# Optimization experiments

Measured on AMD Instinct MI355X. Metric: run time of the kernel, lower is better.

## Reference

```python
import jax, jax.numpy as jnp
import numpy as np

B, S, D_IN, D_H = 8, 2048, 512, 512

def setup_inputs() -> dict:
    key = jax.random.key(0)
    ks = jax.random.split(key, 7)
    scale = 1.0 / np.sqrt(D_IN)
    return {
        "x": jax.random.normal(ks[0], (B, S, D_IN), dtype=jnp.float32),
        "Wq": jax.random.uniform(ks[1], (D_IN, D_H), jnp.float32, -scale, scale),
        "bq": jax.random.uniform(ks[2], (D_H,), jnp.float32, -scale, scale),
        "Wk": jax.random.uniform(ks[3], (D_IN, D_H), jnp.float32, -scale, scale),
        "bk": jax.random.uniform(ks[4], (D_H,), jnp.float32, -scale, scale),
        "Wv": jax.random.uniform(ks[5], (D_IN, D_H), jnp.float32, -scale, scale),
        "bv": jax.random.uniform(ks[6], (D_H,), jnp.float32, -scale, scale),
    }

def reference(x, Wq, bq, Wk, bk, Wv, bv):
    q = jnp.einsum("bsd,dh->bsh", x, Wq) + bq  # [B,S,H]
    k = jnp.einsum("bsd,dh->bsh", x, Wk) + bk
    v = jnp.einsum("bsd,dh->bsh", x, Wv) + bv
    # NOTE: original has NO 1/sqrt(d) scaling — faithful reproduction
    scores = jnp.einsum("bqh,bkh->bqk", q, k)  # [B,S,S]
    probs = jax.nn.softmax(scores, axis=-1)
    return jnp.einsum("bqk,bkh->bqh", probs, v)
```

## Files before the change

kernel.cpp:

```cpp
#include <hip/hip_runtime.h>


typedef __attribute__((ext_vector_type(8))) _Float16 f16x8;
typedef __attribute__((ext_vector_type(8))) short bf16x8;
typedef __attribute__((ext_vector_type(4))) float f32x4;

__device__ __forceinline__ unsigned short f2h(float f) {
  _Float16 h = (_Float16)f;
  return *(unsigned short*)&h;
}
__device__ __forceinline__ unsigned short f2bf(float f) {
  unsigned int u = __float_as_uint(f);
  unsigned int r = (u + 0x7fffu + ((u >> 16) & 1u)) >> 16;
  return (unsigned short)r;
}
__device__ __forceinline__ float bf2f(unsigned short h) {
  return __uint_as_float(((unsigned int)h) << 16);
}

__device__ __forceinline__ void load_lds16(const void* g, void* l) {
  __builtin_amdgcn_global_load_lds(
      (const __attribute__((address_space(1))) unsigned int*)g,
      (__attribute__((address_space(3))) unsigned int*)l, 16, 0, 0);
}

__global__ __launch_bounds__(256) void convx_kernel(const float* __restrict__ x,
                                                    unsigned short* __restrict__ xh) {
  int i = blockIdx.x * 256 + threadIdx.x;
  float4 v = ((const float4*)x)[i];
  union { unsigned short h[4]; short4 s4; } u;
  u.h[0] = f2h(v.x); u.h[1] = f2h(v.y); u.h[2] = f2h(v.z); u.h[3] = f2h(v.w);
  ((short4*)xh)[i] = u.s4;
}

__global__ __launch_bounds__(256) void convw_kernel(
    const float* __restrict__ W0, const float* __restrict__ W1,
    const float* __restrict__ W2, unsigned short* __restrict__ Wt) {
  const float* W = (blockIdx.z == 0) ? W0 : (blockIdx.z == 1) ? W1 : W2;
  unsigned short* t = Wt + (size_t)blockIdx.z * 512 * 512;
  __shared__ float tile[32][33];
  int tx = threadIdx.x, ty = threadIdx.y;
  int h0 = blockIdx.x * 32, d0 = blockIdx.y * 32;
  for (int i = ty; i < 32; i += 8) tile[i][tx] = W[(long)(d0 + i) * 512 + h0 + tx];
  __syncthreads();
  for (int i = ty; i < 32; i += 8)
    t[(long)(h0 + i) * 512 + d0 + tx] = f2h(tile[tx][i]);
}

__global__ __launch_bounds__(256) void gemm_qkv_kernel(
    const unsigned short* __restrict__ A,
    const unsigned short* __restrict__ Bt,
    unsigned short* __restrict__ Qo, unsigned short* __restrict__ Ko,
    unsigned short* __restrict__ VTo,
    const float* __restrict__ bq, const float* __restrict__ bk,
    const float* __restrict__ bv) {
  __shared__ alignas(16) unsigned short As[128 * 32];
  __shared__ alignas(16) unsigned short Bs[128 * 32];
  const int t = threadIdx.x;
  const long long bm = (long long)blockIdx.x * 128;
  const long long bn = (long long)blockIdx.y * 128;

  const int ar = t >> 2;
  const int ac = (t & 3) * 8;

  f32x4 acc[4][4];
#pragma unroll
  for (int i = 0; i < 4; i++)
#pragma unroll
    for (int j = 0; j < 4; j++) acc[i][j] = {0.f, 0.f, 0.f, 0.f};

  const int lane = t & 63;
  const int wave = t >> 6;
  const int wm = (wave & 1) * 64;
  const int wn = (wave >> 1) * 64;
  const int fm = lane & 15;
  const int k8 = (lane >> 4) * 8;

  for (int kt = 0; kt < 512; kt += 32) {
#pragma unroll
    for (int r = 0; r < 2; r++)
      load_lds16(A + (bm + r * 64 + ar) * 512 + kt + ac, &As[r * 2048 + t * 8]);
#pragma unroll
    for (int r = 0; r < 2; r++)
      load_lds16(Bt + (bn + r * 64 + ar) * 512 + kt + ac, &Bs[r * 2048 + t * 8]);
    __syncthreads();

    f16x8 af[4], bfr[4];
#pragma unroll
    for (int i = 0; i < 4; i++)
      af[i] = *(const f16x8*)&As[(wm + i * 16 + fm) * 32 + k8];
#pragma unroll
    for (int j = 0; j < 4; j++)
      bfr[j] = *(const f16x8*)&Bs[(wn + j * 16 + fm) * 32 + k8];
#pragma unroll
    for (int i = 0; i < 4; i++)
#pragma unroll
      for (int j = 0; j < 4; j++)
        acc[i][j] = __builtin_amdgcn_mfma_f32_16x16x32_f16(af[i], bfr[j], acc[i][j], 0, 0, 0);
    __syncthreads();
  }

  const int crow = (lane >> 4) * 4;
  const int ccol = lane & 15;
#pragma unroll
  for (int j = 0; j < 4; j++) {
    const long long col = bn + wn + j * 16 + ccol;
    float bias = (col < 512) ? bq[col] : (col < 1024) ? bk[col - 512] : bv[col - 1024];
#pragma unroll
    for (int i = 0; i < 4; i++) {
      const long long row0 = bm + wm + i * 16 + crow;
      if (col >= 1024) {
        const long long b = row0 >> 11;
        const long long s = row0 & 2047;
        const long long dcol = col - 1024;
        union { unsigned short h[4]; short4 s4; } u;
#pragma unroll
        for (int r = 0; r < 4; r++) u.h[r] = f2bf(acc[i][j][r] + bias);
        const long long unit = b * 64 + (s >> 5);
        const int L = ((int)dcol * 64 + (int)(s & 31) * 2) ^ ((((int)dcol >> 1) & 7) << 4);
        *(short4*)((char*)VTo + unit * 32768 + L) = u.s4;
      } else {
        unsigned short* dst = (col < 512) ? (Qo + row0 * 512 + col)
                                          : (Ko + row0 * 512 + (col - 512));
#pragma unroll
        for (int r = 0; r < 4; r++) dst[(size_t)r * 512] = f2h(acc[i][j][r] + bias);
      }
    }
  }
}

__global__ __launch_bounds__(512, 2) void attn_fused_kernel(
    const unsigned short* __restrict__ Qg,
    const unsigned short* __restrict__ Kg,
    const unsigned short* __restrict__ Vt,
    float* __restrict__ out) {
  __shared__ alignas(16) unsigned short SB[2][16384];
  __shared__ alignas(16) unsigned short Qh[16384];
  __shared__ alignas(16) unsigned short Ps[8192];
  __shared__ float rsw[4][64];

  const int t = threadIdx.x;
  const int lane = t & 63;
  const int w = t >> 6;
  const int fm = lane & 15;
  const int g = lane >> 4;
  const int qh = w & 1;
  const int kg = w >> 1;
  const int b = blockIdx.x & 7;
  const int q0 = (blockIdx.x >> 3) << 6;

  const unsigned short* Qb = Qg + ((size_t)b * 2048 + q0) * 512;
  const unsigned short* Kb = Kg + (size_t)b * 2048 * 512;
  const unsigned short* Vb = Vt + (size_t)b * 2048 * 512;

  int ksrc[4], qsrc[4]; unsigned int sdst[4];
#pragma unroll
  for (int r = 0; r < 4; ++r) {
    const int L = r * 8192 + t * 16;
    sdst[r] = L >> 1;
    const int kr = L >> 8;
    ksrc[r] = kr * 512 + (((L & 255) ^ ((kr & 7) << 4)) >> 1);
    const int qr = L >> 9;
    qsrc[r] = qr * 512 + (((L & 511) ^ ((qr & 7) << 4)) >> 1);
  }

#pragma unroll
  for (int r = 0; r < 4; ++r) load_lds16(Qb + qsrc[r], &SB[0][sdst[r]]);
#pragma unroll
  for (int r = 0; r < 4; ++r) load_lds16(Qb + 256 + qsrc[r], &Qh[sdst[r]]);
  asm volatile("s_waitcnt vmcnt(4)" ::: "memory");
  __builtin_amdgcn_s_barrier();

  const int swz = (fm & 7) << 4;
  const int vswz = ((fm >> 1) & 7) << 4;
  f16x8 qf[2][8];
#pragma unroll
  for (int j = 0; j < 2; ++j)
#pragma unroll
    for (int ds = 0; ds < 8; ++ds)
      qf[j][ds] = *(const f16x8*)((const char*)SB[0] +
          (qh * 32 + j * 16 + fm) * 512 + ((g * 16 + ds * 64) ^ swz));
  asm volatile("s_waitcnt lgkmcnt(0)" ::: "memory");
  __builtin_amdgcn_s_barrier();
#pragma unroll
  for (int r = 0; r < 4; ++r) load_lds16(Kb + ksrc[r], &SB[0][sdst[r]]);

  f32x4 oacc[2][8];
#pragma unroll
  for (int i = 0; i < 2; ++i)
#pragma unroll
    for (int jj = 0; jj < 8; ++jj) oacc[i][jj] = {0.f, 0.f, 0.f, 0.f};
  float psum0 = 0.f, psum1 = 0.f;
  f32x4 sacc[2][2];

  for (int kt = 0; kt < 16; ++kt) {
    const size_t kbase = (size_t)kt * 65536;
#pragma unroll
    for (int u = 0; u < 8; ++u) {
      unsigned short* cur = SB[u & 1];
      unsigned short* nxt = SB[(u & 1) ^ 1];
      if (u < 3) {
#pragma unroll
        for (int r = 0; r < 4; ++r)
          load_lds16(Kb + kbase + (u + 1) * 128 + ksrc[r], &nxt[sdst[r]]);
      } else if (u < 7) {
        const unsigned short* vs = Vb + (size_t)(kt * 4 + (u - 3)) * 16384;
#pragma unroll
        for (int r = 0; r < 4; ++r) load_lds16(vs + sdst[r], &nxt[sdst[r]]);
      } else if (kt < 15) {
#pragma unroll
        for (int r = 0; r < 4; ++r)
          load_lds16(Kb + kbase + 65536 + ksrc[r], &nxt[sdst[r]]);
      }
      if (kt == 15 && u == 7)
        asm volatile("s_waitcnt vmcnt(0)" ::: "memory");
      else
        asm volatile("s_waitcnt vmcnt(4)" ::: "memory");
      __builtin_amdgcn_s_barrier();
      __builtin_amdgcn_sched_barrier(0);

      __builtin_amdgcn_s_setprio(1);
      if (u < 4) {
        if (u == 0) {
          sacc[0][0] = {0.f, 0.f, 0.f, 0.f}; sacc[0][1] = {0.f, 0.f, 0.f, 0.f};
          sacc[1][0] = {0.f, 0.f, 0.f, 0.f}; sacc[1][1] = {0.f, 0.f, 0.f, 0.f};
        }
#pragma unroll
        for (int s = 0; s < 4; ++s) {
          const f16x8 a0 = *(const f16x8*)((const char*)cur +
              (kg * 32 + fm) * 256 + ((g * 16 + s * 64) ^ swz));
          const f16x8 a1 = *(const f16x8*)((const char*)cur +
              (kg * 32 + 16 + fm) * 256 + ((g * 16 + s * 64) ^ swz));
          f16x8 b0, b1;
          if (u < 2) {
            b0 = qf[0][u * 4 + s]; b1 = qf[1][u * 4 + s];
          } else {
            const int dz = (g * 16 + ((u - 2) * 4 + s) * 64) ^ swz;
            b0 = *(const f16x8*)((const char*)Qh + (qh * 32 + fm) * 512 + dz);
            b1 = *(const f16x8*)((const char*)Qh + (qh * 32 + 16 + fm) * 512 + dz);
          }
          sacc[0][0] = __builtin_amdgcn_mfma_f32_16x16x32_f16(a0, b0, sacc[0][0], 0, 0, 0);
          sacc[0][1] = __builtin_amdgcn_mfma_f32_16x16x32_f16(a0, b1, sacc[0][1], 0, 0, 0);
          sacc[1][0] = __builtin_amdgcn_mfma_f32_16x16x32_f16(a1, b0, sacc[1][0], 0, 0, 0);
          sacc[1][1] = __builtin_amdgcn_mfma_f32_16x16x32_f16(a1, b1, sacc[1][1], 0, 0, 0);
        }
        if (u == 3) {
#pragma unroll
          for (int i = 0; i < 2; ++i)
#pragma unroll
            for (int j = 0; j < 2; ++j) {
              const int q = qh * 32 + j * 16 + fm;
              const int k2 = (kg * 32 + i * 16 + g * 4) * 2;
              union { unsigned short h[4]; short4 s4; } uu;
              float s0 = 0.f;
#pragma unroll
              for (int r = 0; r < 4; ++r) {
                const unsigned short pb = f2bf(__expf(sacc[i][j][r]));
                uu.h[r] = pb; s0 += bf2f(pb);
              }
              if (j == 0) psum0 += s0; else psum1 += s0;
              *(short4*)((char*)Ps + q * 256 + (k2 ^ swz)) = uu.s4;
            }
        }
      } else {
        const int ju = u - 4;
        const bf16x8 p0 = *(const bf16x8*)((const char*)Ps +
            (qh * 32 + fm) * 256 + ((ju * 64 + g * 16) ^ swz));
        const bf16x8 p1 = *(const bf16x8*)((const char*)Ps +
            (qh * 32 + 16 + fm) * 256 + ((ju * 64 + g * 16) ^ swz));
#pragma unroll
        for (int jj = 0; jj < 8; ++jj) {
          const bf16x8 vf = *(const bf16x8*)((const char*)cur +
              ((((kg * 128 + jj * 16 + fm) * 64) + g * 16) ^ vswz));
          oacc[0][jj] = __builtin_amdgcn_mfma_f32_16x16x32_bf16(p0, vf, oacc[0][jj], 0, 0, 0);
          oacc[1][jj] = __builtin_amdgcn_mfma_f32_16x16x32_bf16(p1, vf, oacc[1][jj], 0, 0, 0);
        }
      }
      __builtin_amdgcn_s_setprio(0);
      asm volatile("s_waitcnt lgkmcnt(0)" ::: "memory");
      __builtin_amdgcn_s_barrier();
    }
  }

  psum0 += __shfl_xor(psum0, 16); psum0 += __shfl_xor(psum0, 32);
  psum1 += __shfl_xor(psum1, 16); psum1 += __shfl_xor(psum1, 32);
  if (g == 0) {
    rsw[kg][qh * 32 + fm] = psum0;
    rsw[kg][qh * 32 + 16 + fm] = psum1;
  }
  __syncthreads();

  float* ob = out + ((size_t)b * 2048 + q0) * 512;
#pragma unroll
  for (int i = 0; i < 2; ++i) {
    float inv[4];
#pragma unroll
    for (int r = 0; r < 4; ++r) {
      const int q = qh * 32 + i * 16 + g * 4 + r;
      inv[r] = 1.0f / (rsw[0][q] + rsw[1][q] + rsw[2][q] + rsw[3][q]);
    }
#pragma unroll
    for (int jj = 0; jj < 8; ++jj) {
      const int d = kg * 128 + jj * 16 + fm;
#pragma unroll
      for (int r = 0; r < 4; ++r)
        ob[(size_t)(qh * 32 + i * 16 + g * 4 + r) * 512 + d] = oacc[i][jj][r] * inv[r];
    }
  }
}

extern "C" void kernel_launch(void* const* d_in, const int* in_sizes, int n_in,
                              void* d_out, int out_size, void* d_ws, size_t ws_size,
                              hipStream_t stream) {
  const float* x  = (const float*)d_in[0];
  const float* Wq = (const float*)d_in[1];
  const float* bq = (const float*)d_in[2];
  const float* Wk = (const float*)d_in[3];
  const float* bk = (const float*)d_in[4];
  const float* Wv = (const float*)d_in[5];
  const float* bv = (const float*)d_in[6];
  float* out = (float*)d_out;

  const size_t SZ = (size_t)16384 * 512 * 2;
  char* p = (char*)d_ws;
  unsigned short* xh = (unsigned short*)p; p += SZ;
  unsigned short* Wt = (unsigned short*)p; p += (size_t)3 * 512 * 512 * 2;
  unsigned short* Qb = (unsigned short*)p; p += SZ;
  unsigned short* Kb = (unsigned short*)p; p += SZ;
  unsigned short* VT = (unsigned short*)p; p += SZ;

  convx_kernel<<<8192, 256, 0, stream>>>(x, xh);
  convw_kernel<<<dim3(16, 16, 3), dim3(32, 8), 0, stream>>>(Wq, Wk, Wv, Wt);
  gemm_qkv_kernel<<<dim3(128, 12), 256, 0, stream>>>(xh, Wt, Qb, Kb, VT, bq, bk, bv);
  attn_fused_kernel<<<256, 512, 0, stream>>>(Qb, Kb, VT, out);
}
```

Baseline: 246.1 us.

## Double-buffer LDS tiles in QKV GEMM with async prefetch and explicit waitcnt

```diff
diff --git a/kernel.cpp b/kernel.cpp
--- a/kernel.cpp
+++ b/kernel.cpp
@@ -54,8 +54,8 @@
     unsigned short* __restrict__ VTo,
     const float* __restrict__ bq, const float* __restrict__ bk,
     const float* __restrict__ bv) {
-  __shared__ alignas(16) unsigned short As[128 * 32];
-  __shared__ alignas(16) unsigned short Bs[128 * 32];
+  __shared__ alignas(16) unsigned short As[2][4096];
+  __shared__ alignas(16) unsigned short Bs[2][4096];
   const int t = threadIdx.x;
   const long long bm = (long long)blockIdx.x * 128;
   const long long bn = (long long)blockIdx.y * 128;
@@ -76,28 +76,47 @@
   const int fm = lane & 15;
   const int k8 = (lane >> 4) * 8;
 
-  for (int kt = 0; kt < 512; kt += 32) {
-#pragma unroll
-    for (int r = 0; r < 2; r++)
-      load_lds16(A + (bm + r * 64 + ar) * 512 + kt + ac, &As[r * 2048 + t * 8]);
-#pragma unroll
-    for (int r = 0; r < 2; r++)
-      load_lds16(Bt + (bn + r * 64 + ar) * 512 + kt + ac, &Bs[r * 2048 + t * 8]);
-    __syncthreads();
+#pragma unroll
+  for (int r = 0; r < 2; r++)
+    load_lds16(A + (bm + r * 64 + ar) * 512 + ac, &As[0][r * 2048 + t * 8]);
+#pragma unroll
+  for (int r = 0; r < 2; r++)
+    load_lds16(Bt + (bn + r * 64 + ar) * 512 + ac, &Bs[0][r * 2048 + t * 8]);
+
+  for (int ktt = 0; ktt < 16; ++ktt) {
+    const int cur = ktt & 1;
+    const int nxt = cur ^ 1;
+    if (ktt < 15) {
+      const int kc = (ktt + 1) * 32;
+#pragma unroll
+      for (int r = 0; r < 2; r++)
+        load_lds16(A + (bm + r * 64 + ar) * 512 + kc + ac, &As[nxt][r * 2048 + t * 8]);
+#pragma unroll
+      for (int r = 0; r < 2; r++)
+        load_lds16(Bt + (bn + r * 64 + ar) * 512 + kc + ac, &Bs[nxt][r * 2048 + t * 8]);
+      asm volatile("s_waitcnt vmcnt(4)" ::: "memory");
+    } else {
+      asm volatile("s_waitcnt vmcnt(0)" ::: "memory");
+    }
+    __builtin_amdgcn_s_barrier();
+    __builtin_amdgcn_sched_barrier(0);
 
     f16x8 af[4], bfr[4];
 #pragma unroll
     for (int i = 0; i < 4; i++)
-      af[i] = *(const f16x8*)&As[(wm + i * 16 + fm) * 32 + k8];
+      af[i] = *(const f16x8*)&As[cur][(wm + i * 16 + fm) * 32 + k8];
 #pragma unroll
     for (int j = 0; j < 4; j++)
-      bfr[j] = *(const f16x8*)&Bs[(wn + j * 16 + fm) * 32 + k8];
+      bfr[j] = *(const f16x8*)&Bs[cur][(wn + j * 16 + fm) * 32 + k8];
+    __builtin_amdgcn_s_setprio(1);
 #pragma unroll
     for (int i = 0; i < 4; i++)
 #pragma unroll
       for (int j = 0; j < 4; j++)
         acc[i][j] = __builtin_amdgcn_mfma_f32_16x16x32_f16(af[i], bfr[j], acc[i][j], 0, 0, 0);
-    __syncthreads();
+    __builtin_amdgcn_s_setprio(0);
+    asm volatile("s_waitcnt lgkmcnt(0)" ::: "memory");
+    __builtin_amdgcn_s_barrier();
   }
 
   const int crow = (lane >> 4) * 4;
```

After: 233.8 us. 5.0% less time.
